# Performance work log

Measured on AMD Instinct MI355X. Metric: run time of the kernel, lower is better.

The kernel has to match this reference:

```python
import jax, jax.numpy as jnp
import numpy as np

EMBED_DIM = 1024
NUM_HEADS = 16
HEAD_DIM = EMBED_DIM // NUM_HEADS
SCALE = HEAD_DIM ** -0.5
B, L = 1, 4096


def setup_inputs() -> dict:
    key = jax.random.key(0)
    ks = jax.random.split(key, 10)
    init = 1.0 / np.sqrt(EMBED_DIM)  # rough Linear-like init scale
    inp = {
        "hidden_states": jax.random.normal(ks[0], (B, L, EMBED_DIM), dtype=jnp.float32),
        # ToMe token sizes: >= 1 so log(size) is finite
        "size": jax.random.uniform(ks[1], (B, 1, L), dtype=jnp.float32) + 1.0,
        "wq": jax.random.normal(ks[2], (EMBED_DIM, EMBED_DIM), dtype=jnp.float32) * init,
        "bq": jax.random.normal(ks[3], (EMBED_DIM,), dtype=jnp.float32) * init,
        "wk": jax.random.normal(ks[4], (EMBED_DIM, EMBED_DIM), dtype=jnp.float32) * init,
        "bk": jax.random.normal(ks[5], (EMBED_DIM,), dtype=jnp.float32) * init,
        "wv": jax.random.normal(ks[6], (EMBED_DIM, EMBED_DIM), dtype=jnp.float32) * init,
        "bv": jax.random.normal(ks[7], (EMBED_DIM,), dtype=jnp.float32) * init,
        "wo": jax.random.normal(ks[8], (EMBED_DIM, EMBED_DIM), dtype=jnp.float32) * init,
        "bo": jax.random.normal(ks[9], (EMBED_DIM,), dtype=jnp.float32) * init,
    }
    return inp


def reference(hidden_states, size, wq, bq, wk, bk, wv, bv, wo, bo):
    b, t, d = hidden_states.shape
    h, hd = NUM_HEADS, HEAD_DIM

    def heads(x):  # (b, t, d) -> (b, h, t, hd)
        return x.reshape(b, t, h, hd).transpose(0, 2, 1, 3)

    q = heads((hidden_states @ wq.T + bq) * SCALE)
    k = heads(hidden_states @ wk.T + bk)
    v = heads(hidden_states @ wv.T + bv)

    metric = k.mean(axis=1)  # (b, t, hd): per-token key averaged over heads

    logits = jnp.einsum('bhqd,bhkd->bhqk', q, k)
    # size: (b, 1, src) -> log-size bias broadcast over heads and queries
    logits = logits + jnp.log(size)[:, None, :, :]
    probs = jax.nn.softmax(logits, axis=-1)  # dropout p=0 (eval)

    attn = jnp.einsum('bhqk,bhkd->bhqd', probs, v)
    attn = attn.transpose(0, 2, 1, 3).reshape(b, t, d)
    out = attn @ wo.T + bo
    return out, metric
```

## Files before the change

kernel.cpp:

```cpp
#include <hip/hip_runtime.h>

static constexpr int L_SEQ = 4096;
static constexpr int EMBED = 1024;
static constexpr int HEADS = 16;
static constexpr int HD    = 64;

typedef unsigned short ushortT;
typedef __attribute__((ext_vector_type(8)))  short short8;
typedef __attribute__((ext_vector_type(4)))  float f32x4;
typedef __attribute__((ext_vector_type(4)))  unsigned uint4v;

#define LOG2E 1.4426950408889634f

__device__ __forceinline__ ushortT f2bf(float f) {
  unsigned u = __builtin_bit_cast(unsigned, f);
  u += 0x7fffu + ((u >> 16) & 1u);
  return (ushortT)(u >> 16);
}
__device__ __forceinline__ float bf2f(ushortT s) {
  return __builtin_bit_cast(float, ((unsigned)s) << 16);
}
__device__ __forceinline__ unsigned cvtpk(float a, float b) {
  unsigned r;
  asm("v_cvt_pk_bf16_f32 %0, %1, %2" : "=v"(r) : "v"(a), "v"(b));
  return r;
}

#define GLOAD_LDS16(g, l) \
  __builtin_amdgcn_global_load_lds((const __attribute__((address_space(1))) void*)(g), \
                                   (__attribute__((address_space(3))) void*)(l), 16, 0, 0)

__global__ void cast_bf16_k(const float* __restrict__ in, ushortT* __restrict__ out, int n8) {
  int i = blockIdx.x * blockDim.x + threadIdx.x;
  if (i >= n8) return;
  const float4* p = (const float4*)in;
  float4 a = p[2 * i], b = p[2 * i + 1];
  uint4 o;
  o.x = (unsigned)f2bf(a.x) | ((unsigned)f2bf(a.y) << 16);
  o.y = (unsigned)f2bf(a.z) | ((unsigned)f2bf(a.w) << 16);
  o.z = (unsigned)f2bf(b.x) | ((unsigned)f2bf(b.y) << 16);
  o.w = (unsigned)f2bf(b.z) | ((unsigned)f2bf(b.w) << 16);
  ((uint4*)out)[i] = o;
}

__global__ void cast4_bf16_k(const float* __restrict__ a, const float* __restrict__ b,
                             const float* __restrict__ c, const float* __restrict__ d,
                             ushortT* __restrict__ out) {
  int idx = blockIdx.x * blockDim.x + threadIdx.x;
  int w = idx >> 17, i = idx & 131071;
  const float* src = (w == 0) ? a : (w == 1) ? b : (w == 2) ? c : d;
  const float4* p = (const float4*)src;
  float4 x = p[2 * i], y = p[2 * i + 1];
  uint4 o;
  o.x = (unsigned)f2bf(x.x) | ((unsigned)f2bf(x.y) << 16);
  o.y = (unsigned)f2bf(x.z) | ((unsigned)f2bf(x.w) << 16);
  o.z = (unsigned)f2bf(y.x) | ((unsigned)f2bf(y.y) << 16);
  o.w = (unsigned)f2bf(y.z) | ((unsigned)f2bf(y.w) << 16);
  ((uint4*)(out + ((size_t)w << 20)))[i] = o;
}

__global__ void l2size_k(const float* __restrict__ sz, float* __restrict__ l2s, int n) {
  int i = blockIdx.x * blockDim.x + threadIdx.x;
  if (i < n) l2s[i] = __log2f(sz[i]);
}

struct GemmArgs { const ushortT* B; const float* bias; void* dst; int mode; };

__global__ __launch_bounds__(256, 3) void gemm_bt_k(
    const ushortT* __restrict__ A, GemmArgs g0, GemmArgs g1, GemmArgs g2)
{
  constexpr int K = 1024;
  __shared__ __align__(16) ushortT As[128 * 64];
  __shared__ __align__(16) ushortT Bs[128 * 64];

  GemmArgs g = (blockIdx.y == 0) ? g0 : ((blockIdx.y == 1) ? g1 : g2);
  const ushortT* __restrict__ Bw = g.B;

  const int tid = threadIdx.x;
  const int wv = tid >> 6, ln = tid & 63;
  const int nb = blockIdx.x & 7, mb = blockIdx.x >> 3;
  const int m0 = mb * 128, n0 = nb * 128;
  const int wr = wv >> 1, wc = wv & 1;
  const int lrow = ln & 15, lq = ln >> 4;

  const int rstg = wv * 8 + (ln >> 3);
  const int ustg = (ln & 7) ^ (ln >> 3);

  f32x4 acc[4][4] = {};

  for (int kt = 0; kt < K; kt += 64) {
#pragma unroll
    for (int i = 0; i < 4; ++i) {
      int r = i * 32 + rstg;
      GLOAD_LDS16(A  + (size_t)(m0 + r) * K + kt + (ustg << 3), As + i * 2048 + wv * 512);
      GLOAD_LDS16(Bw + (size_t)(n0 + r) * K + kt + (ustg << 3), Bs + i * 2048 + wv * 512);
    }
    __syncthreads();
#pragma unroll
    for (int ks = 0; ks < 2; ++ks) {
      short8 a[4], b[4];
#pragma unroll
      for (int mi = 0; mi < 4; ++mi) {
        int ra = wr * 64 + mi * 16 + lrow;
        int u = (ks * 4 + lq) ^ (ra & 7);
        a[mi] = *(const short8*)(As + ra * 64 + (u << 3));
      }
#pragma unroll
      for (int ni = 0; ni < 4; ++ni) {
        int rb = wc * 64 + ni * 16 + lrow;
        int u = (ks * 4 + lq) ^ (rb & 7);
        b[ni] = *(const short8*)(Bs + rb * 64 + (u << 3));
      }
#pragma unroll
      for (int mi = 0; mi < 4; ++mi)
#pragma unroll
        for (int ni = 0; ni < 4; ++ni)
          acc[mi][ni] = __builtin_amdgcn_mfma_f32_16x16x32_bf16(a[mi], b[ni], acc[mi][ni], 0, 0, 0);
    }
    __syncthreads();
  }

  const int mode = g.mode;
  if (mode <= 1) {
    ushortT* dst = (ushortT*)g.dst;
    const float sc = (mode == 0) ? 0.125f : 1.0f;
#pragma unroll
    for (int ni = 0; ni < 4; ++ni) {
      int n = n0 + wc * 64 + ni * 16 + lrow;
      float bsv = g.bias[n];
      size_t base = ((size_t)(n >> 6) * L_SEQ) * HD + (n & 63);
#pragma unroll
      for (int mi = 0; mi < 4; ++mi)
#pragma unroll
        for (int r = 0; r < 4; ++r) {
          int m = m0 + wr * 64 + mi * 16 + lq * 4 + r;
          dst[base + (size_t)m * HD] = f2bf((acc[mi][ni][r] + bsv) * sc);
        }
    }
  } else if (mode == 2) {
    ushortT* dst = (ushortT*)g.dst;
#pragma unroll
    for (int ni = 0; ni < 4; ++ni) {
      int n = n0 + wc * 64 + ni * 16 + lrow;
      float bsv = g.bias[n];
      size_t base = (size_t)n * L_SEQ;
#pragma unroll
      for (int mi = 0; mi < 4; ++mi)
#pragma unroll
        for (int r = 0; r < 4; ++r) {
          int m = m0 + wr * 64 + mi * 16 + lq * 4 + r;
          dst[base + m] = f2bf(acc[mi][ni][r] + bsv);
        }
    }
  } else {
    float* dst = (float*)g.dst;
#pragma unroll
    for (int ni = 0; ni < 4; ++ni) {
      int n = n0 + wc * 64 + ni * 16 + lrow;
      float bsv = g.bias[n];
#pragma unroll
      for (int mi = 0; mi < 4; ++mi)
#pragma unroll
        for (int r = 0; r < 4; ++r) {
          int m = m0 + wr * 64 + mi * 16 + lq * 4 + r;
          dst[(size_t)m * EMBED + n] = acc[mi][ni][r] + bsv;
        }
    }
  }
}

__global__ __launch_bounds__(256, 2) void attn_k(
    const ushortT* __restrict__ Q,
    const ushortT* __restrict__ Kb,
    const ushortT* __restrict__ Vt,
    const float*   __restrict__ l2s,
    ushortT* __restrict__ O)
{
  __shared__ __align__(16) ushortT Ks[2][64 * 64];
  __shared__ __align__(16) ushortT Vs[2][64 * 64];

  const int id = blockIdx.x;
  const int xcd = id & 7, s = id >> 3;
  const int h  = xcd * 2 + (s >> 5);
  const int q0 = (s & 31) * 128;

  const int tid = threadIdx.x;
  const int wv = tid >> 6, ln = tid & 63;
  const int lrow = ln & 15, lq = ln >> 4;

  short8 qf[2][2];
#pragma unroll
  for (int hf = 0; hf < 2; ++hf) {
    const ushortT* qp = Q + ((size_t)h * L_SEQ + q0 + wv * 32 + hf * 16 + lrow) * HD + lq * 8;
    qf[hf][0] = *(const short8*)qp;
    qf[hf][1] = *(const short8*)(qp + 32);
  }

  f32x4 o0[4] = {}, o1[4] = {};
  float mrun0 = -1e30f, lrun0 = 0.f;
  float mrun1 = -1e30f, lrun1 = 0.f;

  const int rstg = wv * 8 + (ln >> 3);
  const int ustg = (ln & 7) ^ (ln >> 3);

  const ushortT* kbase = Kb + ((size_t)h * L_SEQ + rstg) * HD + (ustg << 3);
  const ushortT* vbase = Vt + ((size_t)(h * HD) + rstg) * L_SEQ + (ustg << 3);

  auto STAGE = [&](int buf, int t0) {
#pragma unroll
    for (int i = 0; i < 2; ++i) {
      GLOAD_LDS16(kbase + t0 * 64 + i * (32 * HD),    &Ks[buf][i * 2048 + wv * 512]);
      GLOAD_LDS16(vbase + t0 + i * (32 * L_SEQ),      &Vs[buf][i * 2048 + wv * 512]);
    }
  };

  const int sw = lrow & 7;
  const int vo0 = lrow * 128 + ((((lq >> 1))     ^ sw) << 4) + (lq & 1) * 8;
  const int vo1 = lrow * 128 + ((((lq >> 1) + 2) ^ sw) << 4) + (lq & 1) * 8;
  const int vo2 = lrow * 128 + ((((lq >> 1) + 4) ^ sw) << 4) + (lq & 1) * 8;
  const int vo3 = lrow * 128 + ((((lq >> 1) + 6) ^ sw) << 4) + (lq & 1) * 8;

  STAGE(0, 0);
  __syncthreads();

  constexpr int NT = L_SEQ / 64;
#pragma unroll 1
  for (int t = 0; t < NT; ++t) {
    const int cur = t & 1;
    if (t + 1 < NT) STAGE(cur ^ 1, (t + 1) * 64);
    const int t0 = t * 64;
    const ushortT* Kt = &Ks[cur][0];
    const char*    Vb = (const char*)&Vs[cur][0];

    f32x4 s0[4] = {}, s1[4] = {};
    __builtin_amdgcn_s_setprio(1);
#pragma unroll
    for (int ks = 0; ks < 2; ++ks) {
#pragma unroll
      for (int f = 0; f < 4; ++f) {
        int key = f * 16 + lrow;
        int u = (ks * 4 + lq) ^ (key & 7);
        short8 kb = *(const short8*)(Kt + key * 64 + (u << 3));
        s0[f] = __builtin_amdgcn_mfma_f32_16x16x32_bf16(kb, qf[0][ks], s0[f], 0, 0, 0);
        s1[f] = __builtin_amdgcn_mfma_f32_16x16x32_bf16(kb, qf[1][ks], s1[f], 0, 0, 0);
      }
    }
    __builtin_amdgcn_s_setprio(0);

#pragma unroll
    for (int f = 0; f < 4; ++f) {
      f32x4 b = *(const f32x4*)(l2s + t0 + f * 16 + lq * 4);
#pragma unroll
      for (int r = 0; r < 4; ++r) {
        s0[f][r] = s0[f][r] * LOG2E + b[r];
        s1[f][r] = s1[f][r] * LOG2E + b[r];
      }
    }

    float pm0 = fmaxf(fmaxf(fmaxf(s0[0][0], s0[0][1]), fmaxf(s0[0][2], s0[0][3])),
                      fmaxf(fmaxf(s0[1][0], s0[1][1]), fmaxf(s0[1][2], s0[1][3])));
    pm0 = fmaxf(pm0, fmaxf(fmaxf(fmaxf(s0[2][0], s0[2][1]), fmaxf(s0[2][2], s0[2][3])),
                           fmaxf(fmaxf(s0[3][0], s0[3][1]), fmaxf(s0[3][2], s0[3][3]))));
    float pm1 = fmaxf(fmaxf(fmaxf(s1[0][0], s1[0][1]), fmaxf(s1[0][2], s1[0][3])),
                      fmaxf(fmaxf(s1[1][0], s1[1][1]), fmaxf(s1[1][2], s1[1][3])));
    pm1 = fmaxf(pm1, fmaxf(fmaxf(fmaxf(s1[2][0], s1[2][1]), fmaxf(s1[2][2], s1[2][3])),
                           fmaxf(fmaxf(s1[3][0], s1[3][1]), fmaxf(s1[3][2], s1[3][3]))));
    pm0 = fmaxf(pm0, __shfl_xor(pm0, 16));
    pm0 = fmaxf(pm0, __shfl_xor(pm0, 32));
    pm1 = fmaxf(pm1, __shfl_xor(pm1, 16));
    pm1 = fmaxf(pm1, __shfl_xor(pm1, 32));
    float mnew0  = fmaxf(mrun0, pm0);
    float mnew1  = fmaxf(mrun1, pm1);
    float alpha0 = __builtin_amdgcn_exp2f(mrun0 - mnew0);
    float alpha1 = __builtin_amdgcn_exp2f(mrun1 - mnew1);
    mrun0 = mnew0; mrun1 = mnew1;

    float rs0 = 0.f, rs1 = 0.f;
#pragma unroll
    for (int f = 0; f < 4; ++f)
#pragma unroll
      for (int r = 0; r < 4; ++r) {
        float pv0 = __builtin_amdgcn_exp2f(s0[f][r] - mrun0);
        float pv1 = __builtin_amdgcn_exp2f(s1[f][r] - mrun1);
        s0[f][r] = pv0; rs0 += pv0;
        s1[f][r] = pv1; rs1 += pv1;
      }
    rs0 += __shfl_xor(rs0, 16);
    rs0 += __shfl_xor(rs0, 32);
    rs1 += __shfl_xor(rs1, 16);
    rs1 += __shfl_xor(rs1, 32);
    lrun0 = lrun0 * alpha0 + rs0;
    lrun1 = lrun1 * alpha1 + rs1;

    if (!__all(alpha0 == 1.0f && alpha1 == 1.0f)) {
#pragma unroll
      for (int df = 0; df < 4; ++df)
#pragma unroll
        for (int r = 0; r < 4; ++r) {
          o0[df][r] *= alpha0;
          o1[df][r] *= alpha1;
        }
    }

    short8 pb00, pb10, pb01, pb11;
    {
      unsigned a0 = cvtpk(s0[0][0], s0[0][1]), a1 = cvtpk(s0[0][2], s0[0][3]);
      unsigned a2 = cvtpk(s0[1][0], s0[1][1]), a3 = cvtpk(s0[1][2], s0[1][3]);
      unsigned a4 = cvtpk(s0[2][0], s0[2][1]), a5 = cvtpk(s0[2][2], s0[2][3]);
      unsigned a6 = cvtpk(s0[3][0], s0[3][1]), a7 = cvtpk(s0[3][2], s0[3][3]);
      pb00 = __builtin_bit_cast(short8, (uint4v){a0, a1, a2, a3});
      pb10 = __builtin_bit_cast(short8, (uint4v){a4, a5, a6, a7});
      unsigned b0 = cvtpk(s1[0][0], s1[0][1]), b1 = cvtpk(s1[0][2], s1[0][3]);
      unsigned b2 = cvtpk(s1[1][0], s1[1][1]), b3 = cvtpk(s1[1][2], s1[1][3]);
      unsigned b4 = cvtpk(s1[2][0], s1[2][1]), b5 = cvtpk(s1[2][2], s1[2][3]);
      unsigned b6 = cvtpk(s1[3][0], s1[3][1]), b7 = cvtpk(s1[3][2], s1[3][3]);
      pb01 = __builtin_bit_cast(short8, (uint4v){b0, b1, b2, b3});
      pb11 = __builtin_bit_cast(short8, (uint4v){b4, b5, b6, b7});
    }

    __builtin_amdgcn_s_setprio(1);
#pragma unroll
    for (int df = 0; df < 4; ++df) {
      const char* vr = Vb + df * 2048;
      uint2 a0 = *(const uint2*)(vr + vo0);
      uint2 a1 = *(const uint2*)(vr + vo1);
      short8 va = __builtin_bit_cast(short8, (uint4v){a0.x, a0.y, a1.x, a1.y});
      o0[df] = __builtin_amdgcn_mfma_f32_16x16x32_bf16(va, pb00, o0[df], 0, 0, 0);
      o1[df] = __builtin_amdgcn_mfma_f32_16x16x32_bf16(va, pb01, o1[df], 0, 0, 0);
      uint2 a2 = *(const uint2*)(vr + vo2);
      uint2 a3 = *(const uint2*)(vr + vo3);
      short8 vb2 = __builtin_bit_cast(short8, (uint4v){a2.x, a2.y, a3.x, a3.y});
      o0[df] = __builtin_amdgcn_mfma_f32_16x16x32_bf16(vb2, pb10, o0[df], 0, 0, 0);
      o1[df] = __builtin_amdgcn_mfma_f32_16x16x32_bf16(vb2, pb11, o1[df], 0, 0, 0);
    }
    __builtin_amdgcn_s_setprio(0);

    __syncthreads();
  }

  float inv0 = 1.0f / lrun0, inv1 = 1.0f / lrun1;
  ushortT* ob0 = O + (size_t)(q0 + wv * 32 + lrow) * EMBED + h * HD;
  ushortT* ob1 = O + (size_t)(q0 + wv * 32 + 16 + lrow) * EMBED + h * HD;
#pragma unroll
  for (int df = 0; df < 4; ++df) {
    uint2 w0, w1;
    w0.x = (unsigned)f2bf(o0[df][0] * inv0) | ((unsigned)f2bf(o0[df][1] * inv0) << 16);
    w0.y = (unsigned)f2bf(o0[df][2] * inv0) | ((unsigned)f2bf(o0[df][3] * inv0) << 16);
    w1.x = (unsigned)f2bf(o1[df][0] * inv1) | ((unsigned)f2bf(o1[df][1] * inv1) << 16);
    w1.y = (unsigned)f2bf(o1[df][2] * inv1) | ((unsigned)f2bf(o1[df][3] * inv1) << 16);
    *(uint2*)(ob0 + df * 16 + lq * 4) = w0;
    *(uint2*)(ob1 + df * 16 + lq * 4) = w1;
  }
}

__global__ void metric_k(const ushortT* __restrict__ Kb, float* __restrict__ out) {
  int idx = blockIdx.x * blockDim.x + threadIdx.x;
  int t = idx >> 3, c8 = idx & 7;
  float acc[8] = {};
#pragma unroll
  for (int h = 0; h < HEADS; ++h) {
    short8 v = *(const short8*)(Kb + ((size_t)h * L_SEQ + t) * HD + c8 * 8);
#pragma unroll
    for (int j = 0; j < 8; ++j) acc[j] += bf2f((ushortT)v[j]);
  }
  float* dst = out + (size_t)t * HD + c8 * 8;
#pragma unroll
  for (int j = 0; j < 8; ++j) dst[j] = acc[j] * (1.0f / 16.0f);
}

extern "C" void kernel_launch(void* const* d_in, const int* in_sizes, int n_in,
                              void* d_out, int out_size, void* d_ws, size_t ws_size,
                              hipStream_t stream) {
  const float* hs = (const float*)d_in[0];
  const float* sz = (const float*)d_in[1];
  const float* wq = (const float*)d_in[2];
  const float* bq = (const float*)d_in[3];
  const float* wk = (const float*)d_in[4];
  const float* bk = (const float*)d_in[5];
  const float* wv = (const float*)d_in[6];
  const float* bv = (const float*)d_in[7];
  const float* wo = (const float*)d_in[8];
  const float* bo = (const float*)d_in[9];

  char* ws = (char*)d_ws;
  ushortT* hs_b = (ushortT*)(ws);
  ushortT* wq_b = (ushortT*)(ws + (8u << 20));
  ushortT* wk_b = wq_b + (1u << 20);
  ushortT* wv_b = wq_b + (2u << 20);
  ushortT* wo_b = wq_b + (3u << 20);
  ushortT* q_b  = (ushortT*)(ws + (16u << 20));
  ushortT* k_b  = (ushortT*)(ws + (24u << 20));
  ushortT* vt_b = (ushortT*)(ws + (32u << 20));
  ushortT* at_b = (ushortT*)(ws + (40u << 20));
  float*   l2s  = (float*)(ws + (48u << 20));

  float* outp    = (float*)d_out;
  float* metricp = outp + (size_t)L_SEQ * EMBED;

  cast_bf16_k<<<L_SEQ * EMBED / 8 / 256, 256, 0, stream>>>(hs, hs_b, L_SEQ * EMBED / 8);
  cast4_bf16_k<<<2048, 256, 0, stream>>>(wq, wk, wv, wo, wq_b);
  l2size_k<<<L_SEQ / 256, 256, 0, stream>>>(sz, l2s, L_SEQ);

  GemmArgs aq{wq_b, bq, (void*)q_b, 0};
  GemmArgs ak{wk_b, bk, (void*)k_b, 1};
  GemmArgs av{wv_b, bv, (void*)vt_b, 2};
  gemm_bt_k<<<dim3(256, 3), 256, 0, stream>>>(hs_b, aq, ak, av);

  metric_k<<<L_SEQ * 8 / 256, 256, 0, stream>>>(k_b, metricp);

  attn_k<<<512, 256, 0, stream>>>(q_b, k_b, vt_b, l2s, at_b);

  GemmArgs ao{wo_b, bo, (void*)outp, 3};
  gemm_bt_k<<<dim3(256, 1), 256, 0, stream>>>(at_b, ao, ao, ao);
}
```

Before: 201.0 us.

## Split attention KV sequence across two wave groups per block with LDS merge

The attention kernel now uses 512 threads per block: two groups of four waves each process half of the key/value sequence for the same 128 queries, with separate double-buffered LDS tiles. At the end, group 1 writes its partial outputs and running max/sum to LDS, and group 0 merges them with rescaling before writing bf16 output. This doubles the waves available per block (512 blocks on 256 CUs) to hide latency and shortens each wave's serial loop, at the cost of twice the LDS, a merge step and tighter register limits from launch_bounds(512,4).

```diff
diff --git a/kernel.cpp b/kernel.cpp
--- a/kernel.cpp
+++ b/kernel.cpp
@@ -169,15 +169,15 @@
   }
 }
 
-__global__ __launch_bounds__(256, 2) void attn_k(
+__global__ __launch_bounds__(512, 4) void attn_k(
     const ushortT* __restrict__ Q,
     const ushortT* __restrict__ Kb,
     const ushortT* __restrict__ Vt,
     const float*   __restrict__ l2s,
     ushortT* __restrict__ O)
 {
-  __shared__ __align__(16) ushortT Ks[2][64 * 64];
-  __shared__ __align__(16) ushortT Vs[2][64 * 64];
+  __shared__ __align__(16) ushortT Ks[2][2][64 * 64];
+  __shared__ __align__(16) ushortT Vs[2][2][64 * 64];
 
   const int id = blockIdx.x;
   const int xcd = id & 7, s = id >> 3;
@@ -185,13 +185,15 @@
   const int q0 = (s & 31) * 128;
 
   const int tid = threadIdx.x;
-  const int wv = tid >> 6, ln = tid & 63;
+  const int wv  = tid >> 6;
+  const int grp = wv >> 2, wvg = wv & 3;
+  const int ln  = tid & 63;
   const int lrow = ln & 15, lq = ln >> 4;
 
   short8 qf[2][2];
 #pragma unroll
   for (int hf = 0; hf < 2; ++hf) {
-    const ushortT* qp = Q + ((size_t)h * L_SEQ + q0 + wv * 32 + hf * 16 + lrow) * HD + lq * 8;
+    const ushortT* qp = Q + ((size_t)h * L_SEQ + q0 + wvg * 32 + hf * 16 + lrow) * HD + lq * 8;
     qf[hf][0] = *(const short8*)qp;
     qf[hf][1] = *(const short8*)(qp + 32);
   }
@@ -200,17 +202,18 @@
   float mrun0 = -1e30f, lrun0 = 0.f;
   float mrun1 = -1e30f, lrun1 = 0.f;
 
-  const int rstg = wv * 8 + (ln >> 3);
+  const int rstg = wvg * 8 + (ln >> 3);
   const int ustg = (ln & 7) ^ (ln >> 3);
 
   const ushortT* kbase = Kb + ((size_t)h * L_SEQ + rstg) * HD + (ustg << 3);
   const ushortT* vbase = Vt + ((size_t)(h * HD) + rstg) * L_SEQ + (ustg << 3);
 
-  auto STAGE = [&](int buf, int t0) {
+  auto STAGE = [&](int buf, int kt) {
+    const int t0 = kt * 64;
 #pragma unroll
     for (int i = 0; i < 2; ++i) {
-      GLOAD_LDS16(kbase + t0 * 64 + i * (32 * HD),    &Ks[buf][i * 2048 + wv * 512]);
-      GLOAD_LDS16(vbase + t0 + i * (32 * L_SEQ),      &Vs[buf][i * 2048 + wv * 512]);
+      GLOAD_LDS16(kbase + t0 * 64 + i * (32 * HD), &Ks[grp][buf][i * 2048 + wvg * 512]);
+      GLOAD_LDS16(vbase + t0 + i * (32 * L_SEQ),   &Vs[grp][buf][i * 2048 + wvg * 512]);
     }
   };
 
@@ -220,17 +223,17 @@
   const int vo2 = lrow * 128 + ((((lq >> 1) + 4) ^ sw) << 4) + (lq & 1) * 8;
   const int vo3 = lrow * 128 + ((((lq >> 1) + 6) ^ sw) << 4) + (lq & 1) * 8;
 
-  STAGE(0, 0);
+  const int tbase = grp * 32;
+  STAGE(0, tbase);
   __syncthreads();
 
-  constexpr int NT = L_SEQ / 64;
 #pragma unroll 1
-  for (int t = 0; t < NT; ++t) {
+  for (int t = 0; t < 32; ++t) {
     const int cur = t & 1;
-    if (t + 1 < NT) STAGE(cur ^ 1, (t + 1) * 64);
-    const int t0 = t * 64;
-    const ushortT* Kt = &Ks[cur][0];
-    const char*    Vb = (const char*)&Vs[cur][0];
+    if (t + 1 < 32) STAGE(cur ^ 1, tbase + t + 1);
+    const int t0 = (tbase + t) * 64;
+    const ushortT* Kt = &Ks[grp][cur][0];
+    const char*    Vb = (const char*)&Vs[grp][cur][0];
 
     f32x4 s0[4] = {}, s1[4] = {};
     __builtin_amdgcn_s_setprio(1);
@@ -338,18 +341,57 @@
     __syncthreads();
   }
 
-  float inv0 = 1.0f / lrun0, inv1 = 1.0f / lrun1;
-  ushortT* ob0 = O + (size_t)(q0 + wv * 32 + lrow) * EMBED + h * HD;
-  ushortT* ob1 = O + (size_t)(q0 + wv * 32 + 16 + lrow) * EMBED + h * HD;
-#pragma unroll
-  for (int df = 0; df < 4; ++df) {
-    uint2 w0, w1;
-    w0.x = (unsigned)f2bf(o0[df][0] * inv0) | ((unsigned)f2bf(o0[df][1] * inv0) << 16);
-    w0.y = (unsigned)f2bf(o0[df][2] * inv0) | ((unsigned)f2bf(o0[df][3] * inv0) << 16);
-    w1.x = (unsigned)f2bf(o1[df][0] * inv1) | ((unsigned)f2bf(o1[df][1] * inv1) << 16);
-    w1.y = (unsigned)f2bf(o1[df][2] * inv1) | ((unsigned)f2bf(o1[df][3] * inv1) << 16);
-    *(uint2*)(ob0 + df * 16 + lq * 4) = w0;
-    *(uint2*)(ob1 + df * 16 + lq * 4) = w1;
+  float* Ob = (float*)&Ks[0][0][0];
+  float* Ml = (float*)&Vs[0][0][0];
+  const int ql0 = wvg * 32 + lrow;
+
+  if (grp == 1) {
+#pragma unroll
+    for (int df = 0; df < 4; ++df) {
+      *(f32x4*)(Ob + ql0 * 64 + df * 16 + lq * 4)        = o0[df];
+      *(f32x4*)(Ob + (ql0 + 16) * 64 + df * 16 + lq * 4) = o1[df];
+    }
+    Ml[ql0 * 2] = mrun0;        Ml[ql0 * 2 + 1] = lrun0;
+    Ml[(ql0 + 16) * 2] = mrun1; Ml[(ql0 + 16) * 2 + 1] = lrun1;
+  }
+  __syncthreads();
+  if (grp == 0) {
+    {
+      float m1 = Ml[ql0 * 2], l1 = Ml[ql0 * 2 + 1];
+      float m  = fmaxf(mrun0, m1);
+      float w0 = __builtin_amdgcn_exp2f(mrun0 - m);
+      float w1 = __builtin_amdgcn_exp2f(m1 - m);
+      float inv = 1.0f / (lrun0 * w0 + l1 * w1);
+      ushortT* ob = O + (size_t)(q0 + ql0) * EMBED + h * HD;
+#pragma unroll
+      for (int df = 0; df < 4; ++df) {
+        f32x4 p1 = *(const f32x4*)(Ob + ql0 * 64 + df * 16 + lq * 4);
+        uint2 w;
+        w.x = (unsigned)f2bf((o0[df][0] * w0 + p1[0] * w1) * inv) |
+              ((unsigned)f2bf((o0[df][1] * w0 + p1[1] * w1) * inv) << 16);
+        w.y = (unsigned)f2bf((o0[df][2] * w0 + p1[2] * w1) * inv) |
+              ((unsigned)f2bf((o0[df][3] * w0 + p1[3] * w1) * inv) << 16);
+        *(uint2*)(ob + df * 16 + lq * 4) = w;
+      }
+    }
+    {
+      float m1 = Ml[(ql0 + 16) * 2], l1 = Ml[(ql0 + 16) * 2 + 1];
+      float m  = fmaxf(mrun1, m1);
+      float w0 = __builtin_amdgcn_exp2f(mrun1 - m);
+      float w1 = __builtin_amdgcn_exp2f(m1 - m);
+      float inv = 1.0f / (lrun1 * w0 + l1 * w1);
+      ushortT* ob = O + (size_t)(q0 + ql0 + 16) * EMBED + h * HD;
+#pragma unroll
+      for (int df = 0; df < 4; ++df) {
+        f32x4 p1 = *(const f32x4*)(Ob + (ql0 + 16) * 64 + df * 16 + lq * 4);
+        uint2 w;
+        w.x = (unsigned)f2bf((o1[df][0] * w0 + p1[0] * w1) * inv) |
+              ((unsigned)f2bf((o1[df][1] * w0 + p1[1] * w1) * inv) << 16);
+        w.y = (unsigned)f2bf((o1[df][2] * w0 + p1[2] * w1) * inv) |
+              ((unsigned)f2bf((o1[df][3] * w0 + p1[3] * w1) * inv) << 16);
+        *(uint2*)(ob + df * 16 + lq * 4) = w;
+      }
+    }
   }
 }
 
@@ -408,7 +450,7 @@
 
   metric_k<<<L_SEQ * 8 / 256, 256, 0, stream>>>(k_b, metricp);
 
-  attn_k<<<512, 256, 0, stream>>>(q_b, k_b, vt_b, l2s, at_b);
+  attn_k<<<512, 512, 0, stream>>>(q_b, k_b, vt_b, l2s, at_b);
 
   GemmArgs ao{wo_b, bo, (void*)outp, 3};
   gemm_bt_k<<<dim3(256, 1), 256, 0, stream>>>(at_b, ao, ao, ao);
```

New measurement: 185.3 us. 7.8% less time.
